# Performance work log

Measured on AMD Instinct MI355X. Metric: run time of the kernel, lower is better.

## Reference

```python
import jax, jax.numpy as jnp
import numpy as np

N = 200000   # nodes per branch
E = 600000   # directed edges per branch
G = 8192     # graphs per batch
F_IN = 7
H = 128
OUT = 2
BN_EPS = 1e-5


def setup_inputs() -> dict:
    key = jax.random.key(0)
    ks = jax.random.split(key, 16)
    s = 0.05
    inp = {
        "x_c": jax.random.normal(ks[0], (N, F_IN), jnp.float32),
        "edge_index_c": jax.random.randint(ks[1], (2, E), 0, N, jnp.int32),
        "batch_c": jnp.sort(jax.random.randint(ks[2], (N,), 0, G, jnp.int32)),
        "x_s": jax.random.normal(ks[3], (N, F_IN), jnp.float32),
        "edge_index_s": jax.random.randint(ks[4], (2, E), 0, N, jnp.int32),
        "batch_s": jnp.sort(jax.random.randint(ks[5], (N,), 0, G, jnp.int32)),
        "Wc0": jax.random.normal(ks[6], (F_IN, H), jnp.float32) * s,
        "bc0": jnp.zeros((H,), jnp.float32),
        "Wc1": jax.random.normal(ks[7], (H, H), jnp.float32) * s,
        "bc1": jnp.zeros((H,), jnp.float32),
        "bnc_gamma": jnp.ones((2, H), jnp.float32),
        "bnc_beta": jnp.zeros((2, H), jnp.float32),
        "bnc_mean": jax.random.normal(ks[8], (2, H), jnp.float32) * 0.01,
        "bnc_var": jnp.ones((2, H), jnp.float32),
        "Ws0": jax.random.normal(ks[9], (F_IN, H), jnp.float32) * s,
        "bs0": jnp.zeros((H,), jnp.float32),
        "Ws1": jax.random.normal(ks[10], (H, H), jnp.float32) * s,
        "bs1": jnp.zeros((H,), jnp.float32),
        "bns_gamma": jnp.ones((2, H), jnp.float32),
        "bns_beta": jnp.zeros((2, H), jnp.float32),
        "bns_mean": jax.random.normal(ks[11], (2, H), jnp.float32) * 0.01,
        "bns_var": jnp.ones((2, H), jnp.float32),
        "fc1_w": jax.random.normal(ks[12], (2 * H, H), jnp.float32) * s,
        "fc1_b": jnp.zeros((H,), jnp.float32),
        "fc2_w": jax.random.normal(ks[13], (H, OUT), jnp.float32) * s,
        "fc2_b": jnp.zeros((OUT,), jnp.float32),
        "num_graphs": G,
    }
    return inp


def _gcn_conv(x, src, dst, W, b):
    """PyG GCNConv: D^{-1/2}(A+I)D^{-1/2} X W + b, self-loops added."""
    n = x.shape[0]
    h = x @ W                                   # [n, H]
    loop = jnp.arange(n, dtype=src.dtype)
    src2 = jnp.concatenate([src, loop])
    dst2 = jnp.concatenate([dst, loop])
    deg = jax.ops.segment_sum(jnp.ones_like(dst2, h.dtype), dst2, num_segments=n)
    dinv = jnp.where(deg > 0, jax.lax.rsqrt(deg), 0.0)
    coef = (dinv[src2] * dinv[dst2])[:, None]   # [E+n, 1]
    out = jax.ops.segment_sum(h[src2] * coef, dst2, num_segments=n)
    return out + b


def _branch(x, ei, W0, b0, W1, b1, gamma, beta, mean, var):
    src, dst = ei[0], ei[1]
    for i, (W, b) in enumerate(((W0, b0), (W1, b1))):
        x = _gcn_conv(x, src, dst, W, b)
        # BatchNorm1d (eval mode) + ReLU; dropout is identity in eval
        x = (x - mean[i]) * jax.lax.rsqrt(var[i] + BN_EPS) * gamma[i] + beta[i]
        x = jax.nn.relu(x)
    return x


def _mean_pool(x, batch, num_graphs):
    s = jax.ops.segment_sum(x, batch, num_segments=num_graphs)
    cnt = jax.ops.segment_sum(jnp.ones_like(batch, x.dtype), batch, num_segments=num_graphs)
    return s / jnp.maximum(cnt, 1.0)[:, None]


def reference(x_c, edge_index_c, batch_c, x_s, edge_index_s, batch_s,
              Wc0, bc0, Wc1, bc1, bnc_gamma, bnc_beta, bnc_mean, bnc_var,
              Ws0, bs0, Ws1, bs1, bns_gamma, bns_beta, bns_mean, bns_var,
              fc1_w, fc1_b, fc2_w, fc2_b, num_graphs):
    hc = _branch(x_c, edge_index_c, Wc0, bc0, Wc1, bc1,
                 bnc_gamma, bnc_beta, bnc_mean, bnc_var)
    hs = _branch(x_s, edge_index_s, Ws0, bs0, Ws1, bs1,
                 bns_gamma, bns_beta, bns_mean, bns_var)
    pc = _mean_pool(hc, batch_c, num_graphs)   # [G, H]
    ps = _mean_pool(hs, batch_s, num_graphs)   # [G, H]
    x = jnp.concatenate([pc, ps], axis=1)      # [G, 2H]
    x = jax.nn.relu(x @ fc1_w + fc1_b)
    return x @ fc2_w + fc2_b                   # [G, 2]
```

## Files before the change

kernel.cpp:

```cpp
#include <hip/hip_runtime.h>

#define NN 200000
#define NE 600000
#define NG 8192
#define HD 128
#define FIN 7
#define BN_EPS 1e-5f

#define CHUNK 1024
#define NB 196
#define TA 64
#define NBT (NN / TA)
#define ECAP 320
#define GMAX 8

__global__ void k_hist(const int* __restrict__ dstC, const int* __restrict__ dstS,
                       const int* __restrict__ batchC, const int* __restrict__ batchS,
                       int* __restrict__ degC, int* __restrict__ degS,
                       int* __restrict__ cntC, int* __restrict__ cntS) {
    int e = blockIdx.x * 256 + threadIdx.x;
    if (e < NE)            atomicAdd(&degC[dstC[e]], 1);
    else if (e < 2 * NE)   atomicAdd(&degS[dstS[e - NE]], 1);
    if (e < NN)                      atomicAdd(&cntC[batchC[e]], 1);
    else if (e >= NE && e < NE + NN) atomicAdd(&cntS[batchS[e - NE]], 1);
}

__global__ void k_scan1m(const int* __restrict__ degC, const int* __restrict__ degS,
                         int* __restrict__ bsumC, int* __restrict__ bsumS,
                         float* __restrict__ dinvC, float* __restrict__ dinvS,
                         const float* __restrict__ xC, const float* __restrict__ xS,
                         float* __restrict__ xsC, float* __restrict__ xsS) {
    __shared__ int sd[256];
    int t = threadIdx.x;
    int b = blockIdx.x;
    bool sBr = b >= NB;
    int bb = sBr ? b - NB : b;
    const int* deg = sBr ? degS : degC;
    const float* x = sBr ? xS : xC;
    float* dinv = sBr ? dinvS : dinvC;
    float* xs   = sBr ? xsS : xsC;
    int* bsum = sBr ? bsumS : bsumC;
    int base = bb * CHUNK + t * 4;
    int s = 0;
#pragma unroll
    for (int j = 0; j < 4; j++) {
        int i = base + j;
        if (i < NN) {
            int d = deg[i];
            s += d;
            float di = rsqrtf((float)(d + 1));
            dinv[i] = di;
            float4 v0, v1;
            v0.x = x[(size_t)i * FIN + 0] * di;
            v0.y = x[(size_t)i * FIN + 1] * di;
            v0.z = x[(size_t)i * FIN + 2] * di;
            v0.w = x[(size_t)i * FIN + 3] * di;
            v1.x = x[(size_t)i * FIN + 4] * di;
            v1.y = x[(size_t)i * FIN + 5] * di;
            v1.z = x[(size_t)i * FIN + 6] * di;
            v1.w = 0.f;
            *reinterpret_cast<float4*>(&xs[(size_t)i * 8])     = v0;
            *reinterpret_cast<float4*>(&xs[(size_t)i * 8 + 4]) = v1;
        }
    }
    sd[t] = s; __syncthreads();
    for (int st = 128; st > 0; st >>= 1) { if (t < st) sd[t] += sd[t + st]; __syncthreads(); }
    if (t == 0) bsum[bb] = sd[0];
}

__global__ void k_scan2m(int* __restrict__ bsumC, int* __restrict__ bsumS) {
    __shared__ int sd[256];
    int* bsum = blockIdx.x ? bsumS : bsumC;
    int t = threadIdx.x;
    int v = (t < NB) ? bsum[t] : 0;
    sd[t] = v; __syncthreads();
    for (int st = 1; st < 256; st <<= 1) {
        int add = (t >= st) ? sd[t - st] : 0;
        __syncthreads();
        sd[t] += add;
        __syncthreads();
    }
    if (t < NB) bsum[t] = sd[t] - v;
}

__global__ void k_scan3m(const int* __restrict__ degC, const int* __restrict__ degS,
                         const int* __restrict__ bsumC, const int* __restrict__ bsumS,
                         int* __restrict__ offsC, int* __restrict__ offsS,
                         int* __restrict__ curC, int* __restrict__ curS) {
    __shared__ int sd[256];
    int t = threadIdx.x;
    int b = blockIdx.x;
    bool sBr = b >= NB;
    int bb = sBr ? b - NB : b;
    const int* deg  = sBr ? degS  : degC;
    const int* bsum = sBr ? bsumS : bsumC;
    int* offs   = sBr ? offsS : offsC;
    int* cursor = sBr ? curS  : curC;
    int base = bb * CHUNK + t * 4;
    int v[4]; int s = 0;
#pragma unroll
    for (int j = 0; j < 4; j++) { int i = base + j; v[j] = (i < NN) ? deg[i] : 0; s += v[j]; }
    sd[t] = s; __syncthreads();
    for (int st = 1; st < 256; st <<= 1) {
        int add = (t >= st) ? sd[t - st] : 0;
        __syncthreads();
        sd[t] += add;
        __syncthreads();
    }
    int run = bsum[bb] + sd[t] - s;
#pragma unroll
    for (int j = 0; j < 4; j++) {
        int i = base + j;
        if (i < NN) { offs[i] = run; cursor[i] = run; run += v[j]; }
    }
    if (bb == 0 && t == 0) offs[NN] = NE;
}

__global__ void k_fillm(const int* __restrict__ srcC, const int* __restrict__ dstC,
                        const int* __restrict__ srcS, const int* __restrict__ dstS,
                        int* __restrict__ curC, int* __restrict__ curS,
                        int* __restrict__ csrC, int* __restrict__ csrS) {
    int e = blockIdx.x * 256 + threadIdx.x;
    if (e < NE) {
        int d = dstC[e];
        int pos = atomicAdd(&curC[d], 1);
        csrC[pos] = srcC[e];
    } else if (e < 2 * NE) {
        int ee = e - NE;
        int d = dstS[ee];
        int pos = atomicAdd(&curS[d], 1);
        csrS[pos] = srcS[ee];
    }
}

__global__ void k_aggxm(const float* __restrict__ xsC, const float* __restrict__ xsS,
                        const float* __restrict__ dinvC, const float* __restrict__ dinvS,
                        const int* __restrict__ offsC, const int* __restrict__ offsS,
                        const int* __restrict__ csrC, const int* __restrict__ csrS,
                        float* __restrict__ axdC, float* __restrict__ axdS) {
    int gid = blockIdx.x * 256 + threadIdx.x;
    bool sBr = gid >= NN * 8;
    int lid = sBr ? gid - NN * 8 : gid;
    const float* xs   = sBr ? xsS   : xsC;
    const float* dinv = sBr ? dinvS : dinvC;
    const int*   offs = sBr ? offsS : offsC;
    const int*   csr  = sBr ? csrS  : csrC;
    float*       axd  = sBr ? axdS  : axdC;
    int i = lid >> 3, f = lid & 7;
    float v = xs[lid];
    int o1 = offs[i], o2 = offs[i + 1];
    int j = o1;
    for (; j + 2 <= o2; j += 2) {
        int s0 = csr[j], s1 = csr[j + 1];
        float u0 = xs[(size_t)s0 * 8 + f];
        float u1 = xs[(size_t)s1 * 8 + f];
        v += u0; v += u1;
    }
    if (j < o2) v += xs[(size_t)csr[j] * 8 + f];
    float di = dinv[i];
    axd[lid] = (f == 7) ? di : v * di;
}

__device__ __forceinline__ void src_contrib(float4 r0, float4 r1,
                                            const float4* wp, const float4 c4, float4& a) {
    float axr[7] = { r0.x, r0.y, r0.z, r0.w, r1.x, r1.y, r1.z };
    float4 y = c4;
#pragma unroll
    for (int k = 0; k < FIN; k++) {
        y.x = fmaf(axr[k], wp[k].x, y.x);
        y.y = fmaf(axr[k], wp[k].y, y.y);
        y.z = fmaf(axr[k], wp[k].z, y.z);
        y.w = fmaf(axr[k], wp[k].w, y.w);
    }
    a.x = fmaf(fmaxf(y.x, 0.f), r1.w, a.x);
    a.y = fmaf(fmaxf(y.y, 0.f), r1.w, a.y);
    a.z = fmaf(fmaxf(y.z, 0.f), r1.w, a.z);
    a.w = fmaf(fmaxf(y.w, 0.f), r1.w, a.w);
}

__global__ __launch_bounds__(256, 4) void k_agp2(
    const float* __restrict__ axdC, const float* __restrict__ axdS,
    const int* __restrict__ offsC, const int* __restrict__ offsS,
    const int* __restrict__ csrC, const int* __restrict__ csrS,
    const int* __restrict__ batchC, const int* __restrict__ batchS,
    const float* __restrict__ Wc0, const float* __restrict__ bc0,
    const float* __restrict__ bncG, const float* __restrict__ bncB,
    const float* __restrict__ bncM, const float* __restrict__ bncV,
    const float* __restrict__ Wc1, const float* __restrict__ bc1,
    const float* __restrict__ Ws0, const float* __restrict__ bs0,
    const float* __restrict__ bnsG, const float* __restrict__ bnsB,
    const float* __restrict__ bnsM, const float* __restrict__ bnsV,
    const float* __restrict__ Ws1, const float* __restrict__ bs1,
    float* __restrict__ poolC, float* __restrict__ poolS)
{
    __shared__ float g2[TA][HD];
    __shared__ float spool[GMAX * HD];
    __shared__ int soffs[TA + 1];
    __shared__ int scsr[ECAP];
    int b = blockIdx.x;
    bool sBr = b >= NBT;
    int bb = sBr ? b - NBT : b;
    const float* axd  = sBr ? axdS  : axdC;
    const int*  offs  = sBr ? offsS : offsC;
    const int*  csr   = sBr ? csrS  : csrC;
    const int*  batch = sBr ? batchS : batchC;
    const float* W0   = sBr ? Ws0 : Wc0;
    const float* b0   = sBr ? bs0 : bc0;
    const float* bnG  = sBr ? bnsG : bncG;
    const float* bnB  = sBr ? bnsB : bncB;
    const float* bnM  = sBr ? bnsM : bncM;
    const float* bnV  = sBr ? bnsV : bncV;
    const float* W1   = sBr ? Ws1 : Wc1;
    const float* b1   = sBr ? bs1 : bc1;
    float* pool       = sBr ? poolS : poolC;

    int t = threadIdx.x;
    int nbase = bb * TA;
    if (t <= TA) soffs[t] = offs[nbase + t];
#pragma unroll
    for (int r = 0; r < GMAX * HD / 256; r++) spool[r * 256 + t] = 0.f;
    __syncthreads();
    int E0 = soffs[0], E1 = soffs[TA];
    int ecap = (E1 - E0) < ECAP ? (E1 - E0) : ECAP;
    for (int j = t; j < ecap; j += 256) scsr[j] = csr[E0 + j];

    int q = t & 31, ng = t >> 5;
    int f4 = q * 4, n0 = ng * 8;

    float4 gm = *reinterpret_cast<const float4*>(&bnG[f4]);
    float4 vr = *reinterpret_cast<const float4*>(&bnV[f4]);
    float4 mn = *reinterpret_cast<const float4*>(&bnM[f4]);
    float4 bt = *reinterpret_cast<const float4*>(&bnB[f4]);
    float4 bb0 = *reinterpret_cast<const float4*>(&b0[f4]);
    float4 gsc;
    gsc.x = gm.x * rsqrtf(vr.x + BN_EPS);
    gsc.y = gm.y * rsqrtf(vr.y + BN_EPS);
    gsc.z = gm.z * rsqrtf(vr.z + BN_EPS);
    gsc.w = gm.w * rsqrtf(vr.w + BN_EPS);
    float4 wp[FIN];
#pragma unroll
    for (int k = 0; k < FIN; k++) {
        float4 w = *reinterpret_cast<const float4*>(&W0[k * HD + f4]);
        wp[k] = make_float4(w.x * gsc.x, w.y * gsc.y, w.z * gsc.z, w.w * gsc.w);
    }
    float4 c4 = make_float4((bb0.x - mn.x) * gsc.x + bt.x,
                            (bb0.y - mn.y) * gsc.y + bt.y,
                            (bb0.z - mn.z) * gsc.z + bt.z,
                            (bb0.w - mn.w) * gsc.w + bt.w);
    __syncthreads();

    float sdv8[8];
#pragma unroll
    for (int n = 0; n < 8; n++) {
        int ln = n0 + n;
        float4 a = make_float4(0.f, 0.f, 0.f, 0.f);
        {
            float4 r0 = *reinterpret_cast<const float4*>(&axd[(size_t)(nbase + ln) * 8]);
            float4 r1 = *reinterpret_cast<const float4*>(&axd[(size_t)(nbase + ln) * 8 + 4]);
            sdv8[n] = r1.w;
            src_contrib(r0, r1, wp, c4, a);
        }
        int e = soffs[ln], ee = soffs[ln + 1];
        for (; e < ee; e++) {
            int j = e - E0;
            int s = (j < ECAP) ? scsr[j] : csr[e];
            float4 r0 = *reinterpret_cast<const float4*>(&axd[(size_t)s * 8]);
            float4 r1 = *reinterpret_cast<const float4*>(&axd[(size_t)s * 8 + 4]);
            src_contrib(r0, r1, wp, c4, a);
        }
        *reinterpret_cast<float4*>(&g2[ln][f4]) = a;
    }
    __syncthreads();

    float acc[8][4];
#pragma unroll
    for (int a = 0; a < 8; a++)
#pragma unroll
        for (int c = 0; c < 4; c++) acc[a][c] = 0.f;

    for (int k = 0; k < 128; k += 4) {
        float ha[8][4];
#pragma unroll
        for (int a = 0; a < 8; a++) {
            float4 hv = *reinterpret_cast<const float4*>(&g2[n0 + a][k]);
            ha[a][0] = hv.x; ha[a][1] = hv.y; ha[a][2] = hv.z; ha[a][3] = hv.w;
        }
#pragma unroll
        for (int j = 0; j < 4; j++) {
            float4 w = *reinterpret_cast<const float4*>(&W1[(k + j) * HD + f4]);
#pragma unroll
            for (int a = 0; a < 8; a++) {
                acc[a][0] = fmaf(ha[a][j], w.x, acc[a][0]);
                acc[a][1] = fmaf(ha[a][j], w.y, acc[a][1]);
                acc[a][2] = fmaf(ha[a][j], w.z, acc[a][2]);
                acc[a][3] = fmaf(ha[a][j], w.w, acc[a][3]);
            }
        }
    }

    float4 gm2 = *reinterpret_cast<const float4*>(&bnG[HD + f4]);
    float4 bt2 = *reinterpret_cast<const float4*>(&bnB[HD + f4]);
    float4 mn2 = *reinterpret_cast<const float4*>(&bnM[HD + f4]);
    float4 vr2 = *reinterpret_cast<const float4*>(&bnV[HD + f4]);
    float4 bb1 = *reinterpret_cast<const float4*>(&b1[f4]);
    float Ax = gm2.x * rsqrtf(vr2.x + BN_EPS), Bx = (bb1.x - mn2.x) * Ax + bt2.x;
    float Ay = gm2.y * rsqrtf(vr2.y + BN_EPS), By = (bb1.y - mn2.y) * Ay + bt2.y;
    float Az = gm2.z * rsqrtf(vr2.z + BN_EPS), Bz = (bb1.z - mn2.z) * Az + bt2.z;
    float Aw = gm2.w * rsqrtf(vr2.w + BN_EPS), Bw = (bb1.w - mn2.w) * Aw + bt2.w;

    int gfirst = batch[nbase];
    float sx = 0, sy = 0, sz = 0, sw = 0;
    int curg = -1;
#pragma unroll
    for (int a = 0; a < 8; a++) {
        int i = nbase + n0 + a;
        int g = batch[i];
        float sdv = sdv8[a];
        float zx = fmaxf(fmaf(acc[a][0] * sdv, Ax, Bx), 0.f);
        float zy = fmaxf(fmaf(acc[a][1] * sdv, Ay, By), 0.f);
        float zz = fmaxf(fmaf(acc[a][2] * sdv, Az, Bz), 0.f);
        float zw = fmaxf(fmaf(acc[a][3] * sdv, Aw, Bw), 0.f);
        if (g != curg) {
            if (curg >= 0) {
                int slot = curg - gfirst;
                if (slot < GMAX) {
                    atomicAdd(&spool[slot * HD + f4 + 0], sx);
                    atomicAdd(&spool[slot * HD + f4 + 1], sy);
                    atomicAdd(&spool[slot * HD + f4 + 2], sz);
                    atomicAdd(&spool[slot * HD + f4 + 3], sw);
                } else {
                    atomicAdd(&pool[(size_t)curg * HD + f4 + 0], sx);
                    atomicAdd(&pool[(size_t)curg * HD + f4 + 1], sy);
                    atomicAdd(&pool[(size_t)curg * HD + f4 + 2], sz);
                    atomicAdd(&pool[(size_t)curg * HD + f4 + 3], sw);
                }
            }
            curg = g; sx = zx; sy = zy; sz = zz; sw = zw;
        } else { sx += zx; sy += zy; sz += zz; sw += zw; }
    }
    {
        int slot = curg - gfirst;
        if (slot < GMAX) {
            atomicAdd(&spool[slot * HD + f4 + 0], sx);
            atomicAdd(&spool[slot * HD + f4 + 1], sy);
            atomicAdd(&spool[slot * HD + f4 + 2], sz);
            atomicAdd(&spool[slot * HD + f4 + 3], sw);
        } else {
            atomicAdd(&pool[(size_t)curg * HD + f4 + 0], sx);
            atomicAdd(&pool[(size_t)curg * HD + f4 + 1], sy);
            atomicAdd(&pool[(size_t)curg * HD + f4 + 2], sz);
            atomicAdd(&pool[(size_t)curg * HD + f4 + 3], sw);
        }
    }
    __syncthreads();

    int glast = batch[nbase + TA - 1];
    int nslots = glast - gfirst + 1;
    if (nslots > GMAX) nslots = GMAX;
    for (int idx = t; idx < (nslots << 7); idx += 256) {
        atomicAdd(&pool[(size_t)(gfirst + (idx >> 7)) * HD + (idx & 127)], spool[idx]);
    }
}

#define GPB 4
__global__ __launch_bounds__(128) void k_mlp(
    const float* __restrict__ pc, const float* __restrict__ ps,
    const int* __restrict__ cc, const int* __restrict__ cs,
    const float* __restrict__ w1, const float* __restrict__ b1,
    const float* __restrict__ w2, const float* __restrict__ b2,
    float* __restrict__ outp)
{
    __shared__ float xc[GPB][256];
    __shared__ float hb[GPB][128];
    int t = threadIdx.x;
    int g0 = blockIdx.x * GPB;
#pragma unroll
    for (int gg = 0; gg < GPB; gg++) {
        int g = g0 + gg;
        xc[gg][t]       = pc[g * HD + t] / fmaxf((float)cc[g], 1.f);
        xc[gg][128 + t] = ps[g * HD + t] / fmaxf((float)cs[g], 1.f);
    }
    __syncthreads();
    float acc[GPB];
#pragma unroll
    for (int gg = 0; gg < GPB; gg++) acc[gg] = b1[t];
#pragma unroll 4
    for (int k = 0; k < 256; k++) {
        float w = w1[k * HD + t];
#pragma unroll
        for (int gg = 0; gg < GPB; gg++) acc[gg] = fmaf(xc[gg][k], w, acc[gg]);
    }
#pragma unroll
    for (int gg = 0; gg < GPB; gg++) hb[gg][t] = fmaxf(acc[gg], 0.f);
    __syncthreads();
    if (t < GPB * 2) {
        int gg = t >> 1, o = t & 1;
        float v = b2[o];
        for (int k = 0; k < 128; k++) v = fmaf(hb[gg][k], w2[k * 2 + o], v);
        outp[(size_t)(g0 + gg) * 2 + o] = v;
    }
}

extern "C" void kernel_launch(void* const* d_in, const int* in_sizes, int n_in,
                              void* d_out, int out_size, void* d_ws, size_t ws_size,
                              hipStream_t stream) {
    const float* x_c      = (const float*)d_in[0];
    const int*   ei_c     = (const int*)  d_in[1];
    const int*   batch_c  = (const int*)  d_in[2];
    const float* x_s      = (const float*)d_in[3];
    const int*   ei_s     = (const int*)  d_in[4];
    const int*   batch_s  = (const int*)  d_in[5];
    const float* Wc0      = (const float*)d_in[6];
    const float* bc0      = (const float*)d_in[7];
    const float* Wc1      = (const float*)d_in[8];
    const float* bc1      = (const float*)d_in[9];
    const float* bnc_g    = (const float*)d_in[10];
    const float* bnc_b    = (const float*)d_in[11];
    const float* bnc_m    = (const float*)d_in[12];
    const float* bnc_v    = (const float*)d_in[13];
    const float* Ws0      = (const float*)d_in[14];
    const float* bs0      = (const float*)d_in[15];
    const float* Ws1      = (const float*)d_in[16];
    const float* bs1      = (const float*)d_in[17];
    const float* bns_g    = (const float*)d_in[18];
    const float* bns_b    = (const float*)d_in[19];
    const float* bns_m    = (const float*)d_in[20];
    const float* bns_v    = (const float*)d_in[21];
    const float* fc1_w    = (const float*)d_in[22];
    const float* fc1_b    = (const float*)d_in[23];
    const float* fc2_w    = (const float*)d_in[24];
    const float* fc2_b    = (const float*)d_in[25];

    char* p = (char*)d_ws;
    auto take = [&](size_t bytes) {
        void* r = (void*)p;
        p += (bytes + 255) & ~(size_t)255;
        return r;
    };
    float* xs_c   = (float*)take((size_t)NN * 8 * 4);
    float* xs_s   = (float*)take((size_t)NN * 8 * 4);
    float* axd_c  = (float*)take((size_t)NN * 8 * 4);
    float* axd_s  = (float*)take((size_t)NN * 8 * 4);
    int*   deg_c  = (int*)  take((size_t)NN * 4);
    int*   deg_s  = (int*)  take((size_t)NN * 4);
    float* dinv_c = (float*)take((size_t)NN * 4);
    float* dinv_s = (float*)take((size_t)NN * 4);
    int*   offs_c = (int*)  take((size_t)(NN + 1) * 4);
    int*   offs_s = (int*)  take((size_t)(NN + 1) * 4);
    int*   cur_c  = (int*)  take((size_t)NN * 4);
    int*   cur_s  = (int*)  take((size_t)NN * 4);
    int*   csr_c  = (int*)  take((size_t)NE * 4);
    int*   csr_s  = (int*)  take((size_t)NE * 4);
    int*   bsum_c = (int*)  take((size_t)NB * 4);
    int*   bsum_s = (int*)  take((size_t)NB * 4);
    float* pool_c = (float*)take((size_t)NG * HD * 4);
    float* pool_s = (float*)take((size_t)NG * HD * 4);
    int*   cnt_c  = (int*)  take((size_t)NG * 4);
    int*   cnt_s  = (int*)  take((size_t)NG * 4);
    (void)ws_size; (void)in_sizes; (void)n_in; (void)out_size;

    hipMemsetAsync(deg_c, 0, (size_t)2 * NN * 4, stream);
    hipMemsetAsync(pool_c, 0, ((size_t)2 * NG * HD + 2 * NG) * 4, stream);

    const int* src_c = ei_c;           const int* dst_c = ei_c + NE;
    const int* src_s = ei_s;           const int* dst_s = ei_s + NE;

    k_hist  <<<(2 * NE + 255) / 256, 256, 0, stream>>>(dst_c, dst_s, batch_c, batch_s,
                                                       deg_c, deg_s, cnt_c, cnt_s);
    k_scan1m<<<2 * NB, 256, 0, stream>>>(deg_c, deg_s, bsum_c, bsum_s, dinv_c, dinv_s,
                                         x_c, x_s, xs_c, xs_s);
    k_scan2m<<<2, 256, 0, stream>>>(bsum_c, bsum_s);
    k_scan3m<<<2 * NB, 256, 0, stream>>>(deg_c, deg_s, bsum_c, bsum_s,
                                         offs_c, offs_s, cur_c, cur_s);
    k_fillm <<<(2 * NE + 255) / 256, 256, 0, stream>>>(src_c, dst_c, src_s, dst_s,
                                                       cur_c, cur_s, csr_c, csr_s);
    k_aggxm <<<2 * NN * 8 / 256, 256, 0, stream>>>(xs_c, xs_s, dinv_c, dinv_s,
                                                   offs_c, offs_s, csr_c, csr_s, axd_c, axd_s);

    k_agp2<<<2 * NBT, 256, 0, stream>>>(axd_c, axd_s,
                                        offs_c, offs_s, csr_c, csr_s, batch_c, batch_s,
                                        Wc0, bc0, bnc_g, bnc_b, bnc_m, bnc_v, Wc1, bc1,
                                        Ws0, bs0, bns_g, bns_b, bns_m, bns_v, Ws1, bs1,
                                        pool_c, pool_s);

    k_mlp<<<NG / GPB, 128, 0, stream>>>(pool_c, pool_s, cnt_c, cnt_s,
                                        fc1_w, fc1_b, fc2_w, fc2_b, (float*)d_out);
}
```

Baseline: 511.1 us.

## Shrink node tile to 40 and software-pipeline neighbor feature loads in aggregation

The per-block node tile drops from 64 to 40 nodes (5 per thread group instead of 8), giving 5000 blocks instead of 3125 and a smaller register and shared-memory footprint, which should raise occupancy. The edge-aggregation loop now loads the next neighbor's features before processing the current ones, so load latency overlaps with the FMA work. The smaller tile means less reuse of W1 per block in the dense matmul, and there is more per-block setup overhead.

```diff
diff --git a/kernel.cpp b/kernel.cpp
--- a/kernel.cpp
+++ b/kernel.cpp
@@ -9,9 +9,10 @@
 
 #define CHUNK 1024
 #define NB 196
-#define TA 64
+#define TA 40
+#define NPG 5
 #define NBT (NN / TA)
-#define ECAP 320
+#define ECAP 224
 #define GMAX 8
 
 __global__ void k_hist(const int* __restrict__ dstC, const int* __restrict__ dstS,
@@ -225,7 +226,7 @@
     for (int j = t; j < ecap; j += 256) scsr[j] = csr[E0 + j];
 
     int q = t & 31, ng = t >> 5;
-    int f4 = q * 4, n0 = ng * 8;
+    int f4 = q * 4, n0 = ng * NPG;
 
     float4 gm = *reinterpret_cast<const float4*>(&bnG[f4]);
     float4 vr = *reinterpret_cast<const float4*>(&bnV[f4]);
@@ -249,39 +250,38 @@
                             (bb0.w - mn.w) * gsc.w + bt.w);
     __syncthreads();
 
-    float sdv8[8];
-#pragma unroll
-    for (int n = 0; n < 8; n++) {
+    float sdvN[NPG];
+#pragma unroll
+    for (int n = 0; n < NPG; n++) {
         int ln = n0 + n;
         float4 a = make_float4(0.f, 0.f, 0.f, 0.f);
-        {
-            float4 r0 = *reinterpret_cast<const float4*>(&axd[(size_t)(nbase + ln) * 8]);
-            float4 r1 = *reinterpret_cast<const float4*>(&axd[(size_t)(nbase + ln) * 8 + 4]);
-            sdv8[n] = r1.w;
-            src_contrib(r0, r1, wp, c4, a);
-        }
         int e = soffs[ln], ee = soffs[ln + 1];
+        float4 p0 = *reinterpret_cast<const float4*>(&axd[(size_t)(nbase + ln) * 8]);
+        float4 p1 = *reinterpret_cast<const float4*>(&axd[(size_t)(nbase + ln) * 8 + 4]);
+        sdvN[n] = p1.w;
         for (; e < ee; e++) {
             int j = e - E0;
             int s = (j < ECAP) ? scsr[j] : csr[e];
-            float4 r0 = *reinterpret_cast<const float4*>(&axd[(size_t)s * 8]);
-            float4 r1 = *reinterpret_cast<const float4*>(&axd[(size_t)s * 8 + 4]);
-            src_contrib(r0, r1, wp, c4, a);
+            float4 q0 = *reinterpret_cast<const float4*>(&axd[(size_t)s * 8]);
+            float4 q1 = *reinterpret_cast<const float4*>(&axd[(size_t)s * 8 + 4]);
+            src_contrib(p0, p1, wp, c4, a);
+            p0 = q0; p1 = q1;
         }
+        src_contrib(p0, p1, wp, c4, a);
         *reinterpret_cast<float4*>(&g2[ln][f4]) = a;
     }
     __syncthreads();
 
-    float acc[8][4];
-#pragma unroll
-    for (int a = 0; a < 8; a++)
+    float acc[NPG][4];
+#pragma unroll
+    for (int a = 0; a < NPG; a++)
 #pragma unroll
         for (int c = 0; c < 4; c++) acc[a][c] = 0.f;
 
     for (int k = 0; k < 128; k += 4) {
-        float ha[8][4];
-#pragma unroll
-        for (int a = 0; a < 8; a++) {
+        float ha[NPG][4];
+#pragma unroll
+        for (int a = 0; a < NPG; a++) {
             float4 hv = *reinterpret_cast<const float4*>(&g2[n0 + a][k]);
             ha[a][0] = hv.x; ha[a][1] = hv.y; ha[a][2] = hv.z; ha[a][3] = hv.w;
         }
@@ -289,7 +289,7 @@
         for (int j = 0; j < 4; j++) {
             float4 w = *reinterpret_cast<const float4*>(&W1[(k + j) * HD + f4]);
 #pragma unroll
-            for (int a = 0; a < 8; a++) {
+            for (int a = 0; a < NPG; a++) {
                 acc[a][0] = fmaf(ha[a][j], w.x, acc[a][0]);
                 acc[a][1] = fmaf(ha[a][j], w.y, acc[a][1]);
                 acc[a][2] = fmaf(ha[a][j], w.z, acc[a][2]);
@@ -312,10 +312,10 @@
     float sx = 0, sy = 0, sz = 0, sw = 0;
     int curg = -1;
 #pragma unroll
-    for (int a = 0; a < 8; a++) {
+    for (int a = 0; a < NPG; a++) {
         int i = nbase + n0 + a;
         int g = batch[i];
-        float sdv = sdv8[a];
+        float sdv = sdvN[a];
         float zx = fmaxf(fmaf(acc[a][0] * sdv, Ax, Bx), 0.f);
         float zy = fmaxf(fmaf(acc[a][1] * sdv, Ay, By), 0.f);
         float zz = fmaxf(fmaf(acc[a][2] * sdv, Az, Bz), 0.f);
```

After: 529.9 us. 1.04x slower.
